# Kernel optimization log

Hardware: AMD Instinct MI355X
Metric: run time of the kernel (lower is better)

The kernel has to match this reference:

```python
import jax, jax.numpy as jnp
import numpy as np

B, S, D, H = 4, 2048, 2048, 16
HD = D // H  # 128


def setup_inputs() -> dict:
    key = jax.random.key(0)
    k1, k2, k3 = jax.random.split(key, 3)
    sc = 1.0 / np.sqrt(D)
    return {
        "x": jax.random.normal(k1, (B, S, D), dtype=jnp.float32),
        "W_qkv": jax.random.normal(k2, (D, 3 * D), dtype=jnp.float32) * sc,
        "W_out": jax.random.normal(k3, (D, D), dtype=jnp.float32) * sc,
        "b_out": jnp.zeros((D,), dtype=jnp.float32),
    }


def _rotate_half(t):
    t1, t2 = jnp.split(t, 2, axis=-1)
    return jnp.concatenate([-t2, t1], axis=-1)


def reference(x, W_qkv, W_out, b_out):
    b, s, d = x.shape
    qkv = jnp.einsum('bsd,de->bse', x, W_qkv)  # fused QKV projection
    q, k, v = jnp.split(qkv, 3, axis=-1)
    # [b, h, s, hd]
    q = q.reshape(b, s, H, HD).transpose(0, 2, 1, 3)
    k = k.reshape(b, s, H, HD).transpose(0, 2, 1, 3)
    v = v.reshape(b, s, H, HD).transpose(0, 2, 1, 3)
    # RoPE (NeoX-style half-split), past_kv=None so positions = arange(s)
    pos = jnp.arange(s, dtype=jnp.float32)
    theta = 1.0 / (10000.0 ** (jnp.arange(0, HD, 2, dtype=jnp.float32) / HD))
    angles = pos[:, None] * theta[None, :]           # [s, hd/2]
    cos = jnp.concatenate([jnp.cos(angles)] * 2, -1)  # [s, hd] (repeat halves)
    sin = jnp.concatenate([jnp.sin(angles)] * 2, -1)
    cos = cos[None, None]  # [1,1,s,hd]
    sin = sin[None, None]
    q = q * cos + _rotate_half(q) * sin
    k = k * cos + _rotate_half(k) * sin
    # causal SDPA, scale = 1/sqrt(head_dim)
    scale = 1.0 / jnp.sqrt(jnp.asarray(HD, dtype=q.dtype))
    scores = jnp.einsum('bhqd,bhkd->bhqk', q, k) * scale
    causal = jnp.tril(jnp.ones((s, s), dtype=bool))
    scores = jnp.where(causal[None, None], scores, jnp.finfo(scores.dtype).min)
    attn = jax.nn.softmax(scores, axis=-1)
    out = jnp.einsum('bhqk,bhkd->bhqd', attn, v)
    out = out.transpose(0, 2, 1, 3).reshape(b, s, D)
    return jnp.einsum('bsd,de->bse', out, W_out) + b_out
```

## Files before the change

kernel.cpp:

```cpp
#include <hip/hip_runtime.h>

typedef unsigned short ushort_t;
typedef unsigned int u32;
typedef __attribute__((ext_vector_type(8))) short bf16x8;
typedef __attribute__((ext_vector_type(8))) unsigned short u16x8;
typedef __attribute__((ext_vector_type(4))) float f32x4;

#define B_ 4
#define S_ 2048
#define D_ 2048
#define H_ 16
#define HD_ 128

__device__ __forceinline__ ushort_t f2bf(float f) {
  u32 x = __builtin_bit_cast(u32, f);
  x += 0x7fffu + ((x >> 16) & 1u);
  return (ushort_t)(x >> 16);
}
__device__ __forceinline__ float bf2f(ushort_t u) {
  u32 x = ((u32)u) << 16;
  return __builtin_bit_cast(float, x);
}

#define GLL16(srcp, ldsp)                                            \
  __builtin_amdgcn_global_load_lds(                                  \
      (const __attribute__((address_space(1))) u32*)(srcp),          \
      (__attribute__((address_space(3))) u32*)(ldsp), 16, 0, 0)

struct __align__(8) us4 { ushort_t x, y, z, w; };

__global__ void k_cvt_bf16(const float* __restrict__ in, ushort_t* __restrict__ out, int n) {
  int i = (blockIdx.x * 256 + threadIdx.x) * 4;
  if (i >= n) return;
  float4 v = *(const float4*)(in + i);
  us4 o;
  o.x = f2bf(v.x); o.y = f2bf(v.y); o.z = f2bf(v.z); o.w = f2bf(v.w);
  *(us4*)(out + i) = o;
}

__global__ void k_transpose_bf16(const float* __restrict__ in, ushort_t* __restrict__ out,
                                 int R, int C) {
  __shared__ float ld[32][33];
  int c0 = blockIdx.x * 32, r0 = blockIdx.y * 32;
  int tc = threadIdx.x & 31, tr = threadIdx.x >> 5;
#pragma unroll
  for (int i = 0; i < 4; ++i) {
    int r = tr + i * 8;
    ld[r][tc] = in[(size_t)(r0 + r) * C + c0 + tc];
  }
  __syncthreads();
#pragma unroll
  for (int i = 0; i < 4; ++i) {
    int r = tr + i * 8;
    out[(size_t)(c0 + r) * R + r0 + tc] = f2bf(ld[tc][r]);
  }
}

__global__ void k_rope_tables(float* __restrict__ cost, float* __restrict__ sint) {
  int i = blockIdx.x * 256 + threadIdx.x;
  int s = i >> 6, j = i & 63;
  double th = pow(10000.0, -(double)j / 64.0);
  double a = (double)s * th;
  cost[i] = (float)cos(a);
  sint[i] = (float)sin(a);
}

template <int MODE>
__global__ __launch_bounds__(512) void k_gemm8p(const ushort_t* __restrict__ A,
                                                const ushort_t* __restrict__ Bt,
                                                void* __restrict__ Cout,
                                                const float* __restrict__ bias,
                                                int M, int N, int K) {
  __shared__ __attribute__((aligned(16))) ushort_t As[2][256 * 64];
  __shared__ __attribute__((aligned(16))) ushort_t Bs[2][256 * 64];
  const int tid = threadIdx.x;
  const int w = tid >> 6, l = tid & 63;
  const int lr = l & 15, lg = l >> 4;

  const int cpx = gridDim.x >> 3;
  const int bid = blockIdx.x;
  const int swzid = (bid & 7) * cpx + (bid >> 3);
  const int nbn = N >> 8;
  const size_t m0 = (size_t)(swzid / nbn) * 256;
  const size_t n0 = (size_t)(swzid % nbn) * 256;

  const size_t Kp = (size_t)K * 2;
  const char* Ab = (const char*)A + m0 * Kp;
  const char* Bb = (const char*)Bt + n0 * Kp;

  const int r0 = tid >> 3;
  const int ci16 = (tid & 7) * 16;
  const int sw0 = (((tid & 7) ^ (r0 & 7)) << 4);

#define STG_HALF(gbase, hrow, ldsbase, tcol)                                   \
  {                                                                            \
    GLL16((gbase) + (size_t)((hrow) + r0) * Kp + (tcol) + sw0,                 \
          (char*)(ldsbase) + ((hrow) + r0) * 128 + ci16);                      \
    GLL16((gbase) + (size_t)((hrow) + r0 + 64) * Kp + (tcol) +                 \
              (((tid & 7) ^ ((r0 + 64) & 7)) << 4),                            \
          (char*)(ldsbase) + ((hrow) + r0 + 64) * 128 + ci16);                 \
  }

  const int cko0 = (((0 * 4 + lg) ^ (lr & 7)) << 4);
  const int cko1 = (((1 * 4 + lg) ^ (lr & 7)) << 4);

  f32x4 acc[16][2] = {};
  const int NT = K >> 6;

  STG_HALF(Ab, 0, As[0], 0);
  STG_HALF(Bb, 0, Bs[0], 0);
  STG_HALF(Bb, 128, Bs[0], 0);
  STG_HALF(Ab, 128, As[0], 0);
  if (w < 4) asm volatile("s_waitcnt vmcnt(4)");
  else       asm volatile("s_waitcnt vmcnt(2)");
  __builtin_amdgcn_sched_barrier(0);
  __builtin_amdgcn_s_barrier();

  bf16x8 bq[2][2];
  for (int t = 0; t < NT; ++t) {
    const int buf = t & 1;
    const char* Ac = (const char*)As[buf];
    const char* Bc = (const char*)Bs[buf];
    const size_t tc1 = (size_t)(t + 1) * 128;
    const bool more = (t + 1 < NT);
#pragma unroll
    for (int p = 0; p < 4; ++p) {
      if (more) {
        if (p == 0) STG_HALF(Ab, 0, As[buf ^ 1], tc1)
        else if (p == 1) STG_HALF(Bb, 0, Bs[buf ^ 1], tc1)
        else if (p == 2) STG_HALF(Bb, 128, Bs[buf ^ 1], tc1)
        else STG_HALF(Ab, 128, As[buf ^ 1], tc1)
      }
      bf16x8 af[4][2];
#pragma unroll
      for (int m = 0; m < 4; ++m) {
        const int row = p * 64 + m * 16 + lr;
        af[m][0] = *(const bf16x8*)(Ac + row * 128 + cko0);
        af[m][1] = *(const bf16x8*)(Ac + row * 128 + cko1);
      }
      if (p == 0) {
#pragma unroll
        for (int n = 0; n < 2; ++n) {
          const int row = w * 32 + n * 16 + lr;
          bq[n][0] = *(const bf16x8*)(Bc + row * 128 + cko0);
          bq[n][1] = *(const bf16x8*)(Bc + row * 128 + cko1);
        }
      }
      __builtin_amdgcn_s_barrier();
      asm volatile("s_waitcnt lgkmcnt(0)");
      __builtin_amdgcn_sched_barrier(0);
      __builtin_amdgcn_s_setprio(1);
#pragma unroll
      for (int m = 0; m < 4; ++m)
#pragma unroll
        for (int n = 0; n < 2; ++n) {
          acc[p * 4 + m][n] =
              __builtin_amdgcn_mfma_f32_16x16x32_bf16(af[m][0], bq[n][0], acc[p * 4 + m][n], 0, 0, 0);
          acc[p * 4 + m][n] =
              __builtin_amdgcn_mfma_f32_16x16x32_bf16(af[m][1], bq[n][1], acc[p * 4 + m][n], 0, 0, 0);
        }
      __builtin_amdgcn_s_setprio(0);
      if (p == 1) {
        if (more) asm volatile("s_waitcnt vmcnt(4)");
        else      asm volatile("s_waitcnt vmcnt(0)");
        __builtin_amdgcn_sched_barrier(0);
      } else if (p == 3 && more) {
        if (w < 4) asm volatile("s_waitcnt vmcnt(4)");
        else       asm volatile("s_waitcnt vmcnt(2)");
        __builtin_amdgcn_sched_barrier(0);
      }
      __builtin_amdgcn_s_barrier();
    }
  }

  if (MODE == 2) {
#pragma unroll
    for (int n = 0; n < 2; ++n) {
      const size_t col = n0 + w * 32 + n * 16 + lr;
      const float bia = bias[col];
#pragma unroll
      for (int mq = 0; mq < 16; ++mq) {
#pragma unroll
        for (int j = 0; j < 4; ++j) {
          const size_t row = m0 + mq * 16 + lg * 4 + j;
          ((float*)Cout)[row * N + col] = acc[mq][n][j] + bia;
        }
      }
    }
  } else {
    ushort_t* Qbase = (ushort_t*)Cout;
#pragma unroll
    for (int n = 0; n < 2; ++n) {
      const int col = (int)n0 + w * 32 + n * 16 + lr;
      const int p3 = col >> 11, rem = col & 2047;
      const int h = rem >> 7, d = rem & 127;
      ushort_t* base = Qbase + (size_t)p3 * 16777216ull + (size_t)h * (S_ * HD_) + d;
#pragma unroll
      for (int mq = 0; mq < 16; ++mq) {
#pragma unroll
        for (int j = 0; j < 4; ++j) {
          const int row = (int)m0 + mq * 16 + lg * 4 + j;
          const int b2 = row >> 11, s = row & 2047;
          base[(size_t)b2 * (H_ * S_ * HD_) + (size_t)s * HD_] = f2bf(acc[mq][n][j]);
        }
      }
    }
  }
#undef STG_HALF
}

__global__ void k_rope2(ushort_t* __restrict__ t8, const float* __restrict__ cost,
                        const float* __restrict__ sint, float qscale) {
  int s0 = blockIdx.x * 32, h = blockIdx.y, b = blockIdx.z;
  int bh = b * H_ + h;
  const int t = threadIdx.x;
  const int sr = t >> 3, dj = (t & 7) * 8;
  const int s = s0 + sr;
  ushort_t* base = t8 + ((size_t)bh * S_ + s) * HD_;
  u16x8 lo = *(const u16x8*)(base + dj);
  u16x8 hi = *(const u16x8*)(base + 64 + dj);
  const float* cs = cost + s * 64 + dj;
  const float* sn = sint + s * 64 + dj;
  u16x8 olo, ohi;
#pragma unroll
  for (int j = 0; j < 8; ++j) {
    float fl = bf2f(lo[j]), fh = bf2f(hi[j]);
    float c = cs[j], sv = sn[j];
    olo[j] = f2bf((fl * c - fh * sv) * qscale);
    ohi[j] = f2bf((fh * c + fl * sv) * qscale);
  }
  *(u16x8*)(base + dj) = olo;
  *(u16x8*)(base + 64 + dj) = ohi;
}

__global__ void k_transT(const ushort_t* __restrict__ src, ushort_t* __restrict__ dst) {
  __shared__ ushort_t ld[32][33];
  int s0 = blockIdx.x * 32, d0 = blockIdx.y * 32, bh = blockIdx.z;
  const ushort_t* S = src + (size_t)bh * S_ * HD_;
  ushort_t* D = dst + (size_t)bh * HD_ * S_;
  const int tid = threadIdx.x;
#pragma unroll
  for (int i = 0; i < 4; ++i) {
    int e = i * 256 + tid;
    int sr = e >> 5, dc = e & 31;
    ld[sr][dc] = S[(size_t)(s0 + sr) * HD_ + d0 + dc];
  }
  __syncthreads();
#pragma unroll
  for (int i = 0; i < 4; ++i) {
    int e = i * 256 + tid;
    int dc = e >> 5, sr = e & 31;
    D[(size_t)(d0 + dc) * S_ + s0 + sr] = ld[sr][dc];
  }
}

__global__ __launch_bounds__(256, 2) void k_attn4(const ushort_t* __restrict__ Q,
                                                  const ushort_t* __restrict__ K,
                                                  const ushort_t* __restrict__ Vt,
                                                  ushort_t* __restrict__ O) {
  __shared__ __attribute__((aligned(16))) ushort_t Ks[2][64 * 128];
  __shared__ __attribute__((aligned(16))) ushort_t Vs[128 * 64];
  __shared__ __attribute__((aligned(16))) ushort_t Pl[8][16 * 72];

  const int id = blockIdx.x;
  const int work = (id & 7) * 128 + (id >> 3);
  const int bh = work >> 4;
  const int qt = 15 - (work & 15);
  const int b = bh >> 4, h = bh & 15;

  const int tid = threadIdx.x;
  const int w = tid >> 6, l = tid & 63;
  const int lr = l & 15, lg = l >> 4;
  const int qb = qt * 128 + w * 32;

  const ushort_t* Qp = Q + (size_t)bh * S_ * HD_;
  const char* Kpb = (const char*)(K + (size_t)bh * S_ * HD_);
  const char* Vpb = (const char*)(Vt + (size_t)bh * HD_ * S_);

  int kr[4], ksz[4], vr[4], vsz[4];
#pragma unroll
  for (int r = 0; r < 4; ++r) {
    int c = r * 256 + tid;
    kr[r] = c >> 4;
    ksz[r] = (((c & 15) ^ (kr[r] & 15)) << 4);
    vr[r] = c >> 3;
    vsz[r] = (((c & 7) ^ (vr[r] & 7)) << 4);
  }

#define STAGE_K(kb_, bufi)                                                       \
  {                                                                              \
    _Pragma("unroll") for (int r = 0; r < 4; ++r)                                \
        GLL16(Kpb + (size_t)((kb_) + kr[r]) * 256 + ksz[r],                      \
              (char*)Ks[bufi] + (size_t)(r * 256 + tid) * 16);                   \
  }
#define STAGE_V(kb_)                                                             \
  {                                                                              \
    _Pragma("unroll") for (int r = 0; r < 4; ++r)                                \
        GLL16(Vpb + (size_t)vr[r] * (S_ * 2) + (size_t)(kb_) * 2 + vsz[r],       \
              (char*)Vs + (size_t)(r * 256 + tid) * 16);                         \
  }

  bf16x8 qf[2][4];
#pragma unroll
  for (int f = 0; f < 2; ++f)
#pragma unroll
    for (int dw = 0; dw < 4; ++dw)
      qf[f][dw] = *(const bf16x8*)(Qp + (size_t)(qb + f * 16 + lr) * HD_ + dw * 32 + lg * 8);

  f32x4 oacc[2][8] = {};
  float mr[2] = {-1e30f, -1e30f};
  float lsum[2] = {0.f, 0.f};
  const int nkt = 2 * qt + 2;

  STAGE_K(0, 0);
  for (int kt = 0; kt < nkt; ++kt) {
    const int kb = kt * 64;
    const int cur = kt & 1;
    const bool morek = (kt + 1 < nkt);
    if (morek) STAGE_K(kb + 64, cur ^ 1);
    STAGE_V(kb);
    if (morek) asm volatile("s_waitcnt vmcnt(8)");
    else       asm volatile("s_waitcnt vmcnt(4)");
    __builtin_amdgcn_sched_barrier(0);
    __builtin_amdgcn_s_barrier();

    const bool live = (kb <= qb + 31);
    f32x4 st[2][4];
    if (live) {
      const char* Kc = (const char*)Ks[cur];
      __builtin_amdgcn_s_setprio(1);
#pragma unroll
      for (int t = 0; t < 4; ++t) {
        bf16x8 kf[4];
#pragma unroll
        for (int dw = 0; dw < 4; ++dw)
          kf[dw] = *(const bf16x8*)(Kc + (t * 16 + lr) * 256 + (((dw * 4 + lg) ^ lr) << 4));
        f32x4 a0 = {}, a1 = {};
#pragma unroll
        for (int dw = 0; dw < 4; ++dw) {
          a0 = __builtin_amdgcn_mfma_f32_16x16x32_bf16(kf[dw], qf[0][dw], a0, 0, 0, 0);
          a1 = __builtin_amdgcn_mfma_f32_16x16x32_bf16(kf[dw], qf[1][dw], a1, 0, 0, 0);
        }
        st[0][t] = a0;
        st[1][t] = a1;
      }
      __builtin_amdgcn_s_setprio(0);

#pragma unroll
      for (int f = 0; f < 2; ++f) {
        const int qg = qb + f * 16 + lr;
        const bool full = (kb + 63) <= (qb + f * 16);
        float tmax = -1e30f;
        if (full) {
#pragma unroll
          for (int t = 0; t < 4; ++t)
#pragma unroll
            for (int j = 0; j < 4; ++j) tmax = fmaxf(tmax, st[f][t][j]);
        } else {
#pragma unroll
          for (int t = 0; t < 4; ++t)
#pragma unroll
            for (int j = 0; j < 4; ++j) {
              int kg = kb + t * 16 + lg * 4 + j;
              float s = (kg > qg) ? -1e30f : st[f][t][j];
              st[f][t][j] = s;
              tmax = fmaxf(tmax, s);
            }
        }
        tmax = fmaxf(tmax, __shfl_xor(tmax, 16, 64));
        tmax = fmaxf(tmax, __shfl_xor(tmax, 32, 64));
        if (!__all(tmax <= mr[f] + 8.f)) {
          float mnew = fmaxf(mr[f], tmax);
          float alpha = exp2f(mr[f] - mnew);
          mr[f] = mnew;
          lsum[f] *= alpha;
          float a0 = __shfl(alpha, lg * 4 + 0, 64);
          float a1 = __shfl(alpha, lg * 4 + 1, 64);
          float a2 = __shfl(alpha, lg * 4 + 2, 64);
          float a3 = __shfl(alpha, lg * 4 + 3, 64);
#pragma unroll
          for (int dt = 0; dt < 8; ++dt) {
            oacc[f][dt][0] *= a0;
            oacc[f][dt][1] *= a1;
            oacc[f][dt][2] *= a2;
            oacc[f][dt][3] *= a3;
          }
        }
        float psum = 0.f;
        ushort_t* Pw = (ushort_t*)Pl[w * 2 + f];
#pragma unroll
        for (int t = 0; t < 4; ++t) {
          float p0 = exp2f(st[f][t][0] - mr[f]);
          float p1 = exp2f(st[f][t][1] - mr[f]);
          float p2 = exp2f(st[f][t][2] - mr[f]);
          float p3 = exp2f(st[f][t][3] - mr[f]);
          psum += (p0 + p1) + (p2 + p3);
          u32 pk0, pk1;
          asm("v_cvt_pk_bf16_f32 %0, %1, %2" : "=v"(pk0) : "v"(p0), "v"(p1));
          asm("v_cvt_pk_bf16_f32 %0, %1, %2" : "=v"(pk1) : "v"(p2), "v"(p3));
          *(u32*)&Pw[lr * 72 + t * 16 + lg * 4] = pk0;
          *(u32*)&Pw[lr * 72 + t * 16 + lg * 4 + 2] = pk1;
        }
        psum += __shfl_xor(psum, 16, 64);
        psum += __shfl_xor(psum, 32, 64);
        lsum[f] += psum;
      }
    }
    if (morek) asm volatile("s_waitcnt vmcnt(4)");
    else       asm volatile("s_waitcnt vmcnt(0)");
    __builtin_amdgcn_sched_barrier(0);
    __builtin_amdgcn_s_barrier();

    if (live) {
      __builtin_amdgcn_s_setprio(1);
#pragma unroll
      for (int kw = 0; kw < 2; ++kw) {
        bf16x8 pa0 = *(const bf16x8*)&Pl[w * 2 + 0][lr * 72 + kw * 32 + lg * 8];
        bf16x8 pa1 = *(const bf16x8*)&Pl[w * 2 + 1][lr * 72 + kw * 32 + lg * 8];
#pragma unroll
        for (int dt = 0; dt < 8; ++dt) {
          bf16x8 vf = *(const bf16x8*)((const char*)Vs + (dt * 16 + lr) * 128 +
                                       (((kw * 4 + lg) ^ (lr & 7)) << 4));
          oacc[0][dt] = __builtin_amdgcn_mfma_f32_16x16x32_bf16(pa0, vf, oacc[0][dt], 0, 0, 0);
          oacc[1][dt] = __builtin_amdgcn_mfma_f32_16x16x32_bf16(pa1, vf, oacc[1][dt], 0, 0, 0);
        }
      }
      __builtin_amdgcn_s_setprio(0);
    }
    __builtin_amdgcn_s_barrier();
  }

#pragma unroll
  for (int f = 0; f < 2; ++f) {
    float l0 = __shfl(lsum[f], lg * 4 + 0, 64);
    float l1 = __shfl(lsum[f], lg * 4 + 1, 64);
    float l2 = __shfl(lsum[f], lg * 4 + 2, 64);
    float l3 = __shfl(lsum[f], lg * 4 + 3, 64);
    float i0 = 1.f / l0, i1 = 1.f / l1, i2 = 1.f / l2, i3 = 1.f / l3;
    ushort_t* Op = O + (size_t)(b * S_ + qb + f * 16) * D_ + h * HD_;
#pragma unroll
    for (int dt = 0; dt < 8; ++dt) {
      Op[(size_t)(lg * 4 + 0) * D_ + dt * 16 + lr] = f2bf(oacc[f][dt][0] * i0);
      Op[(size_t)(lg * 4 + 1) * D_ + dt * 16 + lr] = f2bf(oacc[f][dt][1] * i1);
      Op[(size_t)(lg * 4 + 2) * D_ + dt * 16 + lr] = f2bf(oacc[f][dt][2] * i2);
      Op[(size_t)(lg * 4 + 3) * D_ + dt * 16 + lr] = f2bf(oacc[f][dt][3] * i3);
    }
  }
#undef STAGE_K
#undef STAGE_V
}

extern "C" void kernel_launch(void* const* d_in, const int* in_sizes, int n_in,
                              void* d_out, int out_size, void* d_ws, size_t ws_size,
                              hipStream_t stream) {
  const float* x = (const float*)d_in[0];
  const float* Wqkv = (const float*)d_in[1];
  const float* Wout = (const float*)d_in[2];
  const float* bout = (const float*)d_in[3];
  char* ws = (char*)d_ws;

  ushort_t* xb  = (ushort_t*)(ws + 0);
  ushort_t* Wqt = (ushort_t*)(ws + 33554432ull);
  ushort_t* Qr  = (ushort_t*)(ws + 58720256ull);
  ushort_t* Kr  = (ushort_t*)(ws + 92274688ull);
  ushort_t* Vr  = (ushort_t*)(ws + 125829120ull);
  ushort_t* Vt  = (ushort_t*)(ws + 159383552ull);
  float* cost   = (float*)(ws + 192937984ull);
  float* sint   = (float*)(ws + 193462272ull);

  const int M = B_ * S_;
  const float kSc = 0.08838834764831845f * 1.4426950408889634f;

  k_cvt_bf16<<<dim3((M * D_) / 4 / 256), 256, 0, stream>>>(x, xb, M * D_);
  k_transpose_bf16<<<dim3(3 * D_ / 32, D_ / 32), 256, 0, stream>>>(Wqkv, Wqt, D_, 3 * D_);
  k_rope_tables<<<dim3(S_ * 64 / 256), 256, 0, stream>>>(cost, sint);

  k_gemm8p<1><<<dim3((M / 256) * (3 * D_ / 256)), 512, 0, stream>>>(
      xb, Wqt, Qr, nullptr, M, 3 * D_, D_);

  k_rope2<<<dim3(S_ / 32, H_, B_), 256, 0, stream>>>(Qr, cost, sint, kSc);
  k_rope2<<<dim3(S_ / 32, H_, B_), 256, 0, stream>>>(Kr, cost, sint, 1.0f);
  k_transT<<<dim3(S_ / 32, HD_ / 32, B_ * H_), 256, 0, stream>>>(Vr, Vt);

  k_transpose_bf16<<<dim3(D_ / 32, D_ / 32), 256, 0, stream>>>(Wout, Vr, D_, D_);

  k_attn4<<<dim3((S_ / 128) * B_ * H_), 256, 0, stream>>>(Qr, Kr, Vt, xb );

  k_gemm8p<2><<<dim3((M / 256) * (D_ / 256)), 512, 0, stream>>>(
      xb, Vr, d_out, bout, M, D_, D_);
}
```

Before: 554.5 us.

## Rewrite GEMM as triple-buffered K=32 pipeline with 2x4 warp tiling

Replaces the double-buffered K=64 GEMM with a three-stage LDS ring of K=32 tiles, prefetching two tiles ahead and issuing one barrier per iteration instead of several. Warps are rearranged into a 2x4 grid with 128x64 output tiles each, so each warp loads fewer operand fragments per MFMA and register reuse improves. A new swizzled LDS layout packs two rows per 128-byte line. The aim is to hide global-load latency and cut barrier and LDS traffic. The cost is more loop iterations and shallower MFMA batches between waits.

```diff
diff --git a/kernel.cpp b/kernel.cpp
--- a/kernel.cpp
+++ b/kernel.cpp
@@ -66,16 +66,17 @@
 }
 
 template <int MODE>
-__global__ __launch_bounds__(512) void k_gemm8p(const ushort_t* __restrict__ A,
+__global__ __launch_bounds__(512) void k_gemm3b(const ushort_t* __restrict__ A,
                                                 const ushort_t* __restrict__ Bt,
                                                 void* __restrict__ Cout,
                                                 const float* __restrict__ bias,
                                                 int M, int N, int K) {
-  __shared__ __attribute__((aligned(16))) ushort_t As[2][256 * 64];
-  __shared__ __attribute__((aligned(16))) ushort_t Bs[2][256 * 64];
+  __shared__ __attribute__((aligned(16))) ushort_t As[3][256 * 32];
+  __shared__ __attribute__((aligned(16))) ushort_t Bs[3][256 * 32];
   const int tid = threadIdx.x;
   const int w = tid >> 6, l = tid & 63;
   const int lr = l & 15, lg = l >> 4;
+  const int wm = w >> 2, wn = w & 3;
 
   const int cpx = gridDim.x >> 3;
   const int bid = blockIdx.x;
@@ -88,125 +89,112 @@
   const char* Ab = (const char*)A + m0 * Kp;
   const char* Bb = (const char*)Bt + n0 * Kp;
 
-  const int r0 = tid >> 3;
-  const int ci16 = (tid & 7) * 16;
-  const int sw0 = (((tid & 7) ^ (r0 & 7)) << 4);
-
-#define STG_HALF(gbase, hrow, ldsbase, tcol)                                   \
-  {                                                                            \
-    GLL16((gbase) + (size_t)((hrow) + r0) * Kp + (tcol) + sw0,                 \
-          (char*)(ldsbase) + ((hrow) + r0) * 128 + ci16);                      \
-    GLL16((gbase) + (size_t)((hrow) + r0 + 64) * Kp + (tcol) +                 \
-              (((tid & 7) ^ ((r0 + 64) & 7)) << 4),                            \
-          (char*)(ldsbase) + ((hrow) + r0 + 64) * 128 + ci16);                 \
-  }
-
-  const int cko0 = (((0 * 4 + lg) ^ (lr & 7)) << 4);
-  const int cko1 = (((1 * 4 + lg) ^ (lr & 7)) << 4);
-
-  f32x4 acc[16][2] = {};
-  const int NT = K >> 6;
-
-  STG_HALF(Ab, 0, As[0], 0);
-  STG_HALF(Bb, 0, Bs[0], 0);
-  STG_HALF(Bb, 128, Bs[0], 0);
-  STG_HALF(Ab, 128, As[0], 0);
-  if (w < 4) asm volatile("s_waitcnt vmcnt(4)");
-  else       asm volatile("s_waitcnt vmcnt(2)");
+  const int s1 = tid + 512;
+  const int g0 = tid >> 3, y0 = (tid & 7) ^ (g0 & 7);
+  const int g1 = s1 >> 3, y1 = (s1 & 7) ^ (g1 & 7);
+  const int ra0 = 2 * g0 + (y0 >> 2), cb0 = (y0 & 3) << 4;
+  const int ra1 = 2 * g1 + (y1 >> 2), cb1 = (y1 & 3) << 4;
+
+#define STG3(gb, tk, lb)                                                   \
+  {                                                                        \
+    GLL16((gb) + (size_t)ra0 * Kp + (tk) + cb0, (char*)(lb) + tid * 16);   \
+    GLL16((gb) + (size_t)ra1 * Kp + (tk) + cb1, (char*)(lb) + s1 * 16);    \
+  }
+
+  const int ya = (((lr & 1) * 4 + lg) ^ ((lr >> 1) & 7)) << 4;
+  int aoff[8], boff[4];
+#pragma unroll
+  for (int m = 0; m < 8; ++m)
+    aoff[m] = (wm * 64 + m * 8 + (lr >> 1)) * 128 + ya;
+#pragma unroll
+  for (int n = 0; n < 4; ++n)
+    boff[n] = (wn * 32 + n * 8 + (lr >> 1)) * 128 + ya;
+
+  f32x4 acc[8][4] = {};
+  const int NT = K >> 5;
+
+  STG3(Ab, (size_t)0, As[0]);
+  STG3(Bb, (size_t)0, Bs[0]);
+  STG3(Ab, (size_t)64, As[1]);
+  STG3(Bb, (size_t)64, Bs[1]);
+  asm volatile("s_waitcnt vmcnt(4)");
   __builtin_amdgcn_sched_barrier(0);
   __builtin_amdgcn_s_barrier();
 
-  bf16x8 bq[2][2];
+  int bi = 0;
   for (int t = 0; t < NT; ++t) {
-    const int buf = t & 1;
-    const char* Ac = (const char*)As[buf];
-    const char* Bc = (const char*)Bs[buf];
-    const size_t tc1 = (size_t)(t + 1) * 128;
-    const bool more = (t + 1 < NT);
-#pragma unroll
-    for (int p = 0; p < 4; ++p) {
-      if (more) {
-        if (p == 0) STG_HALF(Ab, 0, As[buf ^ 1], tc1)
-        else if (p == 1) STG_HALF(Bb, 0, Bs[buf ^ 1], tc1)
-        else if (p == 2) STG_HALF(Bb, 128, Bs[buf ^ 1], tc1)
-        else STG_HALF(Ab, 128, As[buf ^ 1], tc1)
-      }
-      bf16x8 af[4][2];
-#pragma unroll
-      for (int m = 0; m < 4; ++m) {
-        const int row = p * 64 + m * 16 + lr;
-        af[m][0] = *(const bf16x8*)(Ac + row * 128 + cko0);
-        af[m][1] = *(const bf16x8*)(Ac + row * 128 + cko1);
-      }
-      if (p == 0) {
-#pragma unroll
-        for (int n = 0; n < 2; ++n) {
-          const int row = w * 32 + n * 16 + lr;
-          bq[n][0] = *(const bf16x8*)(Bc + row * 128 + cko0);
-          bq[n][1] = *(const bf16x8*)(Bc + row * 128 + cko1);
-        }
-      }
-      __builtin_amdgcn_s_barrier();
-      asm volatile("s_waitcnt lgkmcnt(0)");
+    const char* Ac = (const char*)As[bi];
+    const char* Bc = (const char*)Bs[bi];
+    int b2 = bi + 2; if (b2 >= 3) b2 -= 3;
+    const size_t tk2 = (size_t)(t + 2) * 64;
+    const bool more2 = (t + 2 < NT);
+    if (more2) STG3(Ab, tk2, As[b2]);
+    bf16x8 bq[4], af0[4];
+#pragma unroll
+    for (int n = 0; n < 4; ++n) bq[n] = *(const bf16x8*)(Bc + boff[n]);
+#pragma unroll
+    for (int m = 0; m < 4; ++m) af0[m] = *(const bf16x8*)(Ac + aoff[m]);
+    __builtin_amdgcn_s_setprio(1);
+#pragma unroll
+    for (int m = 0; m < 4; ++m)
+#pragma unroll
+      for (int n = 0; n < 4; ++n)
+        acc[m][n] = __builtin_amdgcn_mfma_f32_16x16x32_bf16(af0[m], bq[n], acc[m][n], 0, 0, 0);
+    __builtin_amdgcn_s_setprio(0);
+    if (more2) STG3(Bb, tk2, Bs[b2]);
+    bf16x8 af1[4];
+#pragma unroll
+    for (int m = 0; m < 4; ++m) af1[m] = *(const bf16x8*)(Ac + aoff[m + 4]);
+    __builtin_amdgcn_s_setprio(1);
+#pragma unroll
+    for (int m = 0; m < 4; ++m)
+#pragma unroll
+      for (int n = 0; n < 4; ++n)
+        acc[m + 4][n] = __builtin_amdgcn_mfma_f32_16x16x32_bf16(af1[m], bq[n], acc[m + 4][n], 0, 0, 0);
+    __builtin_amdgcn_s_setprio(0);
+    if (more2) {
+      asm volatile("s_waitcnt vmcnt(4)");
       __builtin_amdgcn_sched_barrier(0);
-      __builtin_amdgcn_s_setprio(1);
-#pragma unroll
-      for (int m = 0; m < 4; ++m)
-#pragma unroll
-        for (int n = 0; n < 2; ++n) {
-          acc[p * 4 + m][n] =
-              __builtin_amdgcn_mfma_f32_16x16x32_bf16(af[m][0], bq[n][0], acc[p * 4 + m][n], 0, 0, 0);
-          acc[p * 4 + m][n] =
-              __builtin_amdgcn_mfma_f32_16x16x32_bf16(af[m][1], bq[n][1], acc[p * 4 + m][n], 0, 0, 0);
-        }
-      __builtin_amdgcn_s_setprio(0);
-      if (p == 1) {
-        if (more) asm volatile("s_waitcnt vmcnt(4)");
-        else      asm volatile("s_waitcnt vmcnt(0)");
-        __builtin_amdgcn_sched_barrier(0);
-      } else if (p == 3 && more) {
-        if (w < 4) asm volatile("s_waitcnt vmcnt(4)");
-        else       asm volatile("s_waitcnt vmcnt(2)");
-        __builtin_amdgcn_sched_barrier(0);
-      }
-      __builtin_amdgcn_s_barrier();
-    }
+    } else if (t == NT - 2) {
+      asm volatile("s_waitcnt vmcnt(0)");
+      __builtin_amdgcn_sched_barrier(0);
+    }
+    __builtin_amdgcn_s_barrier();
+    bi = bi + 1; if (bi >= 3) bi = 0;
   }
 
   if (MODE == 2) {
 #pragma unroll
-    for (int n = 0; n < 2; ++n) {
-      const size_t col = n0 + w * 32 + n * 16 + lr;
+    for (int n = 0; n < 4; ++n) {
+      const size_t col = n0 + wn * 64 + n * 16 + lr;
       const float bia = bias[col];
 #pragma unroll
-      for (int mq = 0; mq < 16; ++mq) {
+      for (int m = 0; m < 8; ++m)
 #pragma unroll
         for (int j = 0; j < 4; ++j) {
-          const size_t row = m0 + mq * 16 + lg * 4 + j;
-          ((float*)Cout)[row * N + col] = acc[mq][n][j] + bia;
-        }
-      }
+          const size_t row = m0 + wm * 128 + m * 16 + lg * 4 + j;
+          ((float*)Cout)[row * N + col] = acc[m][n][j] + bia;
+        }
     }
   } else {
     ushort_t* Qbase = (ushort_t*)Cout;
 #pragma unroll
-    for (int n = 0; n < 2; ++n) {
-      const int col = (int)n0 + w * 32 + n * 16 + lr;
+    for (int n = 0; n < 4; ++n) {
+      const int col = (int)n0 + wn * 64 + n * 16 + lr;
       const int p3 = col >> 11, rem = col & 2047;
       const int h = rem >> 7, d = rem & 127;
       ushort_t* base = Qbase + (size_t)p3 * 16777216ull + (size_t)h * (S_ * HD_) + d;
 #pragma unroll
-      for (int mq = 0; mq < 16; ++mq) {
+      for (int m = 0; m < 8; ++m)
 #pragma unroll
         for (int j = 0; j < 4; ++j) {
-          const int row = (int)m0 + mq * 16 + lg * 4 + j;
-          const int b2 = row >> 11, s = row & 2047;
-          base[(size_t)b2 * (H_ * S_ * HD_) + (size_t)s * HD_] = f2bf(acc[mq][n][j]);
-        }
-      }
-    }
-  }
-#undef STG_HALF
+          const int row = (int)m0 + wm * 128 + m * 16 + lg * 4 + j;
+          const int b2r = row >> 11, s = row & 2047;
+          base[(size_t)b2r * (H_ * S_ * HD_) + (size_t)s * HD_] = f2bf(acc[m][n][j]);
+        }
+    }
+  }
+#undef STG3
 }
 
 __global__ void k_rope2(ushort_t* __restrict__ t8, const float* __restrict__ cost,
@@ -475,7 +463,7 @@
   k_transpose_bf16<<<dim3(3 * D_ / 32, D_ / 32), 256, 0, stream>>>(Wqkv, Wqt, D_, 3 * D_);
   k_rope_tables<<<dim3(S_ * 64 / 256), 256, 0, stream>>>(cost, sint);
 
-  k_gemm8p<1><<<dim3((M / 256) * (3 * D_ / 256)), 512, 0, stream>>>(
+  k_gemm3b<1><<<dim3((M / 256) * (3 * D_ / 256)), 512, 0, stream>>>(
       xb, Wqt, Qr, nullptr, M, 3 * D_, D_);
 
   k_rope2<<<dim3(S_ / 32, H_, B_), 256, 0, stream>>>(Qr, cost, sint, kSc);
@@ -486,6 +474,6 @@
 
   k_attn4<<<dim3((S_ / 128) * B_ * H_), 256, 0, stream>>>(Qr, Kr, Vt, xb );
 
-  k_gemm8p<2><<<dim3((M / 256) * (D_ / 256)), 512, 0, stream>>>(
+  k_gemm3b<2><<<dim3((M / 256) * (D_ / 256)), 512, 0, stream>>>(
       xb, Vr, d_out, bout, M, D_, D_);
 }
```

After: 551.7 us. No clear change (-0.5%).
